# Kernel optimization log

Hardware: AMD Instinct MI355X
Metric: run time of the kernel (lower is better)

The kernel has to match this reference:

```python
import jax, jax.numpy as jnp
import numpy as np

DIM = 1024
HEADS = 16
HEAD_DIM = DIM // HEADS          # 64
ROT_DIM = max(16, HEAD_DIM // 2) # 32 (already even)
B, S = 1, 2048


def _linear_params(key, scale=0.02):
    w = jax.random.normal(key, (DIM, DIM), dtype=jnp.float32) * scale
    b = jnp.zeros((DIM,), dtype=jnp.float32)
    return w, b


def setup_inputs() -> dict:
    key = jax.random.key(0)
    ks = jax.random.split(key, 16)
    real = jax.random.normal(ks[0], (B, S, DIM), dtype=jnp.float32)
    imag = jax.random.normal(ks[1], (B, S, DIM), dtype=jnp.float32)
    Wq_r, bq_r = _linear_params(ks[2])
    Wk_r, bk_r = _linear_params(ks[3])
    Wv_r, bv_r = _linear_params(ks[4])
    Wq_i, bq_i = _linear_params(ks[5])
    Wk_i, bk_i = _linear_params(ks[6])
    Wv_i, bv_i = _linear_params(ks[7])
    Wo_r, bo_r = _linear_params(ks[8])
    Wo_i, bo_i = _linear_params(ks[9])
    phase_shifts = jax.random.normal(ks[10], (HEADS, HEAD_DIM), dtype=jnp.float32) * 0.02
    # entanglement init: 0.8*I + 0.1 on super/sub diagonal + 0.1 corners
    ent = np.eye(HEADS, dtype=np.float32) * 0.8
    ent += np.diag(np.ones(HEADS - 1, dtype=np.float32) * 0.1, k=1)
    ent += np.diag(np.ones(HEADS - 1, dtype=np.float32) * 0.1, k=-1)
    ent[0, -1] = 0.1
    ent[-1, 0] = 0.1
    entanglement_matrix = jnp.asarray(ent)
    exponent = np.arange(0, ROT_DIM, 2, dtype=np.float64) / ROT_DIM
    rotary_freqs = jnp.asarray((10000.0 ** (-exponent)).astype(np.float32))
    return {
        'real': real, 'imag': imag,
        'Wq_r': Wq_r, 'bq_r': bq_r, 'Wk_r': Wk_r, 'bk_r': bk_r,
        'Wv_r': Wv_r, 'bv_r': bv_r, 'Wq_i': Wq_i, 'bq_i': bq_i,
        'Wk_i': Wk_i, 'bk_i': bk_i, 'Wv_i': Wv_i, 'bv_i': bv_i,
        'Wo_r': Wo_r, 'bo_r': bo_r, 'Wo_i': Wo_i, 'bo_i': bo_i,
        'phase_shifts': phase_shifts,
        'entanglement_matrix': entanglement_matrix,
        'rotary_freqs': rotary_freqs,
        'interference_strength': jnp.float32(0.0),
        'attention_temperature': jnp.float32(0.0),
        'circle_epsilon': jnp.float32(-2.0),
    }


def _proj(x, W, b):
    # nn.Linear: x @ W^T + b, then split heads -> [B,H,S,Dh]
    y = x @ W.T + b
    return y.reshape(B, S, HEADS, HEAD_DIM).transpose(0, 2, 1, 3)


def _rope(x, cos, sin):
    # x: [B,H,S,Dh]; interleaved pairs rotated over first ROT_DIM dims
    xr, xp = x[..., :ROT_DIM], x[..., ROT_DIM:]
    x1, x2 = xr[..., 0::2], xr[..., 1::2]          # [B,H,S,ROT_DIM//2]
    o1 = x1 * cos - x2 * sin
    o2 = x1 * sin + x2 * cos
    out = jnp.stack([o1, o2], axis=-1).reshape(x.shape[:-1] + (ROT_DIM,))
    return jnp.concatenate([out, xp], axis=-1)


def reference(real, imag, Wq_r, bq_r, Wk_r, bk_r, Wv_r, bv_r,
              Wq_i, bq_i, Wk_i, bk_i, Wv_i, bv_i,
              Wo_r, bo_r, Wo_i, bo_i,
              phase_shifts, entanglement_matrix, rotary_freqs,
              interference_strength, attention_temperature, circle_epsilon):
    q_r = _proj(real, Wq_r, bq_r)
    k_r = _proj(real, Wk_r, bk_r)
    v_r = _proj(real, Wv_r, bv_r)
    q_i = _proj(imag, Wq_i, bq_i)
    k_i = _proj(imag, Wk_i, bk_i)
    v_i = _proj(imag, Wv_i, bv_i)

    # rotary embeddings
    pos = jnp.arange(S, dtype=jnp.float32)
    angles = jnp.outer(pos, rotary_freqs)              # [S, ROT_DIM//2]
    cos = jnp.cos(angles)[None, None]                  # [1,1,S,ROT_DIM//2]
    sin = jnp.sin(angles)[None, None]
    q_r = _rope(q_r, cos, sin); k_r = _rope(k_r, cos, sin)
    q_i = _rope(q_i, cos, sin); k_i = _rope(k_i, cos, sin)

    # entanglement mixing across heads
    q_r = jnp.einsum('bhsd,hx->bxsd', q_r, entanglement_matrix)
    q_i = jnp.einsum('bhsd,hx->bxsd', q_i, entanglement_matrix)
    k_r = jnp.einsum('bhsd,hx->bxsd', k_r, entanglement_matrix)
    k_i = jnp.einsum('bhsd,hx->bxsd', k_i, entanglement_matrix)

    # per-head learned phase shift
    pc = jnp.cos(phase_shifts)[None, :, None, :]       # [1,H,1,Dh]
    ps = jnp.sin(phase_shifts)[None, :, None, :]
    q_r, q_i = q_r * pc - q_i * ps, q_r * ps + q_i * pc
    k_r, k_i = k_r * pc - k_i * ps, k_r * ps + k_i * pc

    # complex attention scores (Karatsuba, as in HAKMEMComplexOperations)
    scale = 1.0 / np.sqrt(HEAD_DIM)
    k1 = jnp.einsum('bhsd,bhtd->bhst', q_r, k_r)
    k2 = jnp.einsum('bhsd,bhtd->bhst', q_i, k_i)
    k3 = jnp.einsum('bhsd,bhtd->bhst', q_r + q_i, k_r + k_i)
    attn_r = (k1 - k2) * scale
    attn_i = (k3 - k1 - k2) * scale

    eps = jax.nn.sigmoid(circle_epsilon) * 0.03
    ar = attn_r + eps * attn_i
    ai = attn_i - eps * attn_r
    attn_mag = jnp.sqrt(ar * ar + ai * ai + 1e-6)

    causal = jnp.triu(jnp.ones((S, S), dtype=bool), k=1)[None, None]
    attn_mag = jnp.where(causal, -jnp.inf, attn_mag)

    temp = jnp.clip(jnp.exp(attention_temperature), 0.1, None)
    strength = jax.nn.sigmoid(interference_strength)
    attn = jax.nn.softmax(attn_mag * strength / temp, axis=-1)
    attn = jnp.nan_to_num(attn)

    # complex_matmul(attn, 0, v_r, v_i) -> (attn@v_r, attn@v_i)
    out_r = jnp.einsum('bhst,bhtd->bhsd', attn, v_r)
    out_i = jnp.einsum('bhst,bhtd->bhsd', attn, v_i)
    out_r = out_r.transpose(0, 2, 1, 3).reshape(B, S, DIM)
    out_i = out_i.transpose(0, 2, 1, 3).reshape(B, S, DIM)
    out_r = out_r @ Wo_r.T + bo_r
    out_i = out_i @ Wo_i.T + bo_i
    return out_r, out_i
```

## Files before the change

kernel.cpp:

```cpp
#include <hip/hip_runtime.h>
#include <cstddef>
#include <cstdint>
#include <math.h>

#define S_LEN 2048
#define DIM 1024
#define NH 16
#define HD 64

typedef __attribute__((ext_vector_type(8))) short bf16x8;
typedef __attribute__((ext_vector_type(8))) unsigned short u16x8;
typedef __attribute__((ext_vector_type(4))) float f32x4;

__device__ inline unsigned short f2bf(float x) {
  union { float f; unsigned u; } v; v.f = x;
  unsigned r = v.u + 0x7FFFu + ((v.u >> 16) & 1u);
  return (unsigned short)(r >> 16);
}
__device__ inline float bf2f(unsigned short x) {
  union { unsigned u; float f; } v; v.u = ((unsigned)x) << 16; return v.f;
}

#define GLOAD_LDS16(g, l)                                              \
  __builtin_amdgcn_global_load_lds(                                    \
      (const __attribute__((address_space(1))) void*)(g),              \
      (__attribute__((address_space(3))) void*)(l), 16, 0, 0)

struct ConvBatch {
  const float* src[10];
  unsigned short* dst[10];
  int n[10];
};

__global__ __launch_bounds__(256) void conv_kernel(ConvBatch cb)
{
  const int y = blockIdx.y;
  const int i = (blockIdx.x * 256 + threadIdx.x) * 8;
  if (i >= cb.n[y]) return;
  const float* s = cb.src[y];
  float4 a = *(const float4*)(s + i);
  float4 b = *(const float4*)(s + i + 4);
  u16x8 o;
  o[0] = f2bf(a.x); o[1] = f2bf(a.y); o[2] = f2bf(a.z); o[3] = f2bf(a.w);
  o[4] = f2bf(b.x); o[5] = f2bf(b.y); o[6] = f2bf(b.z); o[7] = f2bf(b.w);
  *(u16x8*)(cb.dst[y] + i) = o;
}

struct BGemm {
  const unsigned short* A[6];
  const unsigned short* W[6];
  const float* bias[6];
  void* C[6];
  int mode[6];
};

__global__ __launch_bounds__(256) void gemm_mfma_kernel(BGemm gb)
{
  constexpr int K = DIM;
  const int z = blockIdx.z;
  const unsigned short* __restrict__ A = gb.A[z];
  const unsigned short* __restrict__ W = gb.W[z];
  const float* __restrict__ bias = gb.bias[z];
  const int mode = gb.mode[z];

  __shared__ __align__(16) unsigned short As[128 * 32];
  __shared__ __align__(16) unsigned short Ws[128 * 32];

  const int t    = threadIdx.x;
  const int lane = t & 63;
  const int w    = t >> 6;
  const int wm   = w >> 1, wn = w & 1;
  const int quad = lane >> 4, lcol = lane & 15;
  const int m0   = blockIdx.y * 128;
  const int n0   = blockIdx.x * 128;

  const int srow = t >> 2;
  const int sk8  = (t & 3) * 8;

  f32x4 acc[4][4];
#pragma unroll
  for (int i = 0; i < 4; i++)
#pragma unroll
    for (int j = 0; j < 4; j++)
#pragma unroll
      for (int r = 0; r < 4; r++) acc[i][j][r] = 0.f;

  for (int k0 = 0; k0 < K; k0 += 32) {
    __syncthreads();
#pragma unroll
    for (int p = 0; p < 2; p++) {
      const unsigned short* ga = A + (size_t)(m0 + p * 64 + srow) * K + k0 + sk8;
      GLOAD_LDS16(ga, As + (size_t)(p * 256 + w * 64) * 8);
      const unsigned short* gw = W + (size_t)(n0 + p * 64 + srow) * K + k0 + sk8;
      GLOAD_LDS16(gw, Ws + (size_t)(p * 256 + w * 64) * 8);
    }
    __syncthreads();

    bf16x8 af[4], bfr[4];
#pragma unroll
    for (int mi = 0; mi < 4; mi++)
      af[mi] = *(const bf16x8*)&As[(wm * 64 + mi * 16 + lcol) * 32 + quad * 8];
#pragma unroll
    for (int ni = 0; ni < 4; ni++)
      bfr[ni] = *(const bf16x8*)&Ws[(wn * 64 + ni * 16 + lcol) * 32 + quad * 8];
#pragma unroll
    for (int mi = 0; mi < 4; mi++)
#pragma unroll
      for (int ni = 0; ni < 4; ni++)
        acc[mi][ni] = __builtin_amdgcn_mfma_f32_16x16x32_bf16(af[mi], bfr[ni], acc[mi][ni], 0, 0, 0);
  }

#pragma unroll
  for (int mi = 0; mi < 4; mi++) {
#pragma unroll
    for (int ni = 0; ni < 4; ni++) {
#pragma unroll
      for (int r = 0; r < 4; r++) {
        const int grow = m0 + wm * 64 + mi * 16 + quad * 4 + r;
        const int gcol = n0 + wn * 64 + ni * 16 + lcol;
        const float v = acc[mi][ni][r] + bias[gcol];
        if (mode == 0) {
          ((float*)gb.C[z])[(size_t)grow * DIM + gcol] = v;
        } else if (mode == 1) {
          const int hh = gcol >> 6, d = gcol & 63;
          ((unsigned short*)gb.C[z])[((size_t)hh * S_LEN + grow) * HD + d] = f2bf(v);
        } else {
          const int hh = gcol >> 6, d = gcol & 63;
          ((unsigned short*)gb.C[z])[((size_t)hh * HD + d) * S_LEN + grow] = f2bf(v);
        }
      }
    }
  }
}

__global__ __launch_bounds__(256) void rope_kernel(
    unsigned short* q_r, unsigned short* k_r,
    unsigned short* q_i, unsigned short* k_i,
    const float* __restrict__ freqs)
{
  const int gid = blockIdx.x * 256 + threadIdx.x;
  const int j  = gid & 15;
  const int s  = (gid >> 4) & (S_LEN - 1);
  const int h  = (gid >> 15) & (NH - 1);
  const int tz = gid >> 19;
  unsigned short* buf = (tz == 0) ? q_r : (tz == 1) ? k_r : (tz == 2) ? q_i : k_i;

  const float ang = (float)s * freqs[j];
  float sn, cs;
  sincosf(ang, &sn, &cs);

  const size_t base = ((size_t)h * S_LEN + s) * HD + 2 * j;
  ushort2 xv = *(const ushort2*)(buf + base);
  const float x1 = bf2f(xv.x), x2 = bf2f(xv.y);
  ushort2 ov;
  ov.x = f2bf(x1 * cs - x2 * sn);
  ov.y = f2bf(x1 * sn + x2 * cs);
  *(ushort2*)(buf + base) = ov;
}

__global__ __launch_bounds__(256) void entangle_kernel(
    const unsigned short* __restrict__ qr_in, const unsigned short* __restrict__ qi_in,
    unsigned short* __restrict__ qr_out, unsigned short* __restrict__ qi_out,
    const unsigned short* __restrict__ kr_in, const unsigned short* __restrict__ ki_in,
    unsigned short* __restrict__ kr_out, unsigned short* __restrict__ ki_out,
    const float* __restrict__ E, const float* __restrict__ phase)
{
  const int z = blockIdx.z;
  const unsigned short* inR = z ? kr_in : qr_in;
  const unsigned short* inI = z ? ki_in : qi_in;
  unsigned short* outR = z ? kr_out : qr_out;
  unsigned short* outI = z ? ki_out : qi_out;

  __shared__ float Es[NH * NH];
  const int t = threadIdx.x;
  Es[t] = E[t];
  __syncthreads();

  const int idx = blockIdx.x * 256 + t;
  const int s = idx >> 6;
  const int d = idx & 63;

  float vr[NH], vi[NH];
#pragma unroll
  for (int h = 0; h < NH; h++) {
    const size_t off = ((size_t)h * S_LEN + s) * HD + d;
    vr[h] = bf2f(inR[off]);
    vi[h] = bf2f(inI[off]);
  }

#pragma unroll
  for (int x = 0; x < NH; x++) {
    float er = 0.f, ei = 0.f;
#pragma unroll
    for (int h = 0; h < NH; h++) {
      const float e = Es[h * NH + x];
      er += vr[h] * e;
      ei += vi[h] * e;
    }
    const float ph = phase[x * HD + d];
    float ps, pc;
    sincosf(ph, &ps, &pc);
    const size_t off = ((size_t)x * S_LEN + s) * HD + d;
    outR[off] = f2bf(er * pc - ei * ps);
    outI[off] = f2bf(er * ps + ei * pc);
  }
}

#define LDK 72

__global__ __launch_bounds__(256) void flash_mfma_kernel(
    const unsigned short* __restrict__ Qr, const unsigned short* __restrict__ Qi,
    const unsigned short* __restrict__ Kr, const unsigned short* __restrict__ Ki,
    const unsigned short* __restrict__ VtR, const unsigned short* __restrict__ VtI,
    unsigned short* __restrict__ Or, unsigned short* __restrict__ Oi,
    const float* __restrict__ p_is, const float* __restrict__ p_at,
    const float* __restrict__ p_ce)
{
  __shared__ __align__(16) unsigned short Krs[64 * LDK];
  __shared__ __align__(16) unsigned short Kis[64 * LDK];
  __shared__ __align__(16) unsigned short VTr[64 * LDK];
  __shared__ __align__(16) unsigned short VTi[64 * LDK];
  __shared__ __align__(16) unsigned short Ps [64 * LDK];

  const int t    = threadIdx.x;
  const int lane = t & 63;
  const int w    = t >> 6;
  const int quad = lane >> 4;
  const int lcol = lane & 15;
  const int h    = blockIdx.y;
  const int itile = 31 - blockIdx.x;
  const int i0   = itile * 64;
  const int ntiles = itile + 1;

  const float strength = 1.f / (1.f + expf(-p_is[0]));
  const float temp     = fmaxf(expf(p_at[0]), 0.1f);
  const float cfac     = strength / temp;
  const float eps      = 0.03f / (1.f + expf(-p_ce[0]));
  const float scale    = 0.125f;

  const int srow = t >> 3;
  const int sd0  = (t & 7) * 8;

  bf16x8 qrf[2], qif[2];
  {
    const int qrow = i0 + w * 16 + lcol;
    const size_t base = ((size_t)h * S_LEN + qrow) * HD;
#pragma unroll
    for (int ks = 0; ks < 2; ks++) {
      qrf[ks] = *(const bf16x8*)(Qr + base + ks * 32 + quad * 8);
      qif[ks] = *(const bf16x8*)(Qi + base + ks * 32 + quad * 8);
    }
  }

  float lsum[4] = {0.f, 0.f, 0.f, 0.f};
  f32x4 aOr[4], aOi[4];
#pragma unroll
  for (int c = 0; c < 4; c++)
#pragma unroll
    for (int r = 0; r < 4; r++) { aOr[c][r] = 0.f; aOi[c][r] = 0.f; }

  bf16x8 pk[2], pki[2], pv[2], pvi[2];

  {
    const size_t kb = ((size_t)h * S_LEN) * HD;
#pragma unroll
    for (int it = 0; it < 2; it++) {
      const int row = srow + it * 32;
      pk [it] = *(const bf16x8*)(Kr  + kb + (size_t)row * HD + sd0);
      pki[it] = *(const bf16x8*)(Ki  + kb + (size_t)row * HD + sd0);
      pv [it] = *(const bf16x8*)(VtR + ((size_t)h * HD + row) * S_LEN + sd0);
      pvi[it] = *(const bf16x8*)(VtI + ((size_t)h * HD + row) * S_LEN + sd0);
    }
  }

  for (int jt = 0; jt < ntiles; jt++) {
    __syncthreads();
#pragma unroll
    for (int it = 0; it < 2; it++) {
      const int row = srow + it * 32;
      *(bf16x8*)&Krs[row * LDK + sd0] = pk [it];
      *(bf16x8*)&Kis[row * LDK + sd0] = pki[it];
      *(bf16x8*)&VTr[row * LDK + sd0] = pv [it];
      *(bf16x8*)&VTi[row * LDK + sd0] = pvi[it];
    }
    __syncthreads();

    if (jt + 1 < ntiles) {
      const int j0n = (jt + 1) * 64;
      const size_t kb = ((size_t)h * S_LEN + j0n) * HD;
#pragma unroll
      for (int it = 0; it < 2; it++) {
        const int row = srow + it * 32;
        pk [it] = *(const bf16x8*)(Kr  + kb + (size_t)row * HD + sd0);
        pki[it] = *(const bf16x8*)(Ki  + kb + (size_t)row * HD + sd0);
        pv [it] = *(const bf16x8*)(VtR + ((size_t)h * HD + row) * S_LEN + j0n + sd0);
        pvi[it] = *(const bf16x8*)(VtI + ((size_t)h * HD + row) * S_LEN + j0n + sd0);
      }
    }

    f32x4 k1[4], k2[4], kx[4];
#pragma unroll
    for (int c = 0; c < 4; c++)
#pragma unroll
      for (int r = 0; r < 4; r++) { k1[c][r] = 0.f; k2[c][r] = 0.f; kx[c][r] = 0.f; }
#pragma unroll
    for (int ks = 0; ks < 2; ks++) {
#pragma unroll
      for (int c = 0; c < 4; c++) {
        const int off = (c * 16 + lcol) * LDK + ks * 32 + quad * 8;
        bf16x8 krf = *(const bf16x8*)&Krs[off];
        bf16x8 kif = *(const bf16x8*)&Kis[off];
        k1[c] = __builtin_amdgcn_mfma_f32_16x16x32_bf16(qrf[ks], krf, k1[c], 0, 0, 0);
        k2[c] = __builtin_amdgcn_mfma_f32_16x16x32_bf16(qif[ks], kif, k2[c], 0, 0, 0);
        kx[c] = __builtin_amdgcn_mfma_f32_16x16x32_bf16(qrf[ks], kif, kx[c], 0, 0, 0);
        kx[c] = __builtin_amdgcn_mfma_f32_16x16x32_bf16(qif[ks], krf, kx[c], 0, 0, 0);
      }
    }

    const bool diag = (jt == ntiles - 1);
    const int j0 = jt * 64;
#pragma unroll
    for (int r = 0; r < 4; r++) {
      const int prow = (w * 16 + quad * 4 + r) * LDK;
      float rs = 0.f;
#pragma unroll
      for (int c = 0; c < 4; c++) {
        const float ar_ = (k1[c][r] - k2[c][r]) * scale;
        const float ai_ = kx[c][r] * scale;
        const float arr = ar_ + eps * ai_;
        const float aii = ai_ - eps * ar_;
        const float mag = sqrtf(arr * arr + aii * aii + 1e-6f);
        float p = __expf(mag * cfac);
        if (diag) {
          const int gi = i0 + w * 16 + quad * 4 + r;
          const int gj = j0 + c * 16 + lcol;
          if (gj > gi) p = 0.f;
        }
        Ps[prow + c * 16 + lcol] = f2bf(p);
        rs += p;
      }
      lsum[r] += rs;
    }

#pragma unroll
    for (int ks = 0; ks < 2; ks++) {
      bf16x8 pf = *(const bf16x8*)&Ps[(w * 16 + lcol) * LDK + ks * 32 + quad * 8];
#pragma unroll
      for (int c = 0; c < 4; c++) {
        const int off = (c * 16 + lcol) * LDK + ks * 32 + quad * 8;
        bf16x8 vrf = *(const bf16x8*)&VTr[off];
        bf16x8 vif = *(const bf16x8*)&VTi[off];
        aOr[c] = __builtin_amdgcn_mfma_f32_16x16x32_bf16(pf, vrf, aOr[c], 0, 0, 0);
        aOi[c] = __builtin_amdgcn_mfma_f32_16x16x32_bf16(pf, vif, aOi[c], 0, 0, 0);
      }
    }
  }

  float inv[4];
#pragma unroll
  for (int r = 0; r < 4; r++) {
    float rs = lsum[r];
#pragma unroll
    for (int off = 1; off < 16; off <<= 1)
      rs += __shfl_xor(rs, off, 16);
    inv[r] = 1.f / rs;
  }

#pragma unroll
  for (int c = 0; c < 4; c++) {
#pragma unroll
    for (int r = 0; r < 4; r++) {
      const int row = i0 + w * 16 + quad * 4 + r;
      const int col = h * HD + c * 16 + lcol;
      Or[(size_t)row * DIM + col] = f2bf(aOr[c][r] * inv[r]);
      Oi[(size_t)row * DIM + col] = f2bf(aOi[c][r] * inv[r]);
    }
  }
}

extern "C" void kernel_launch(void* const* d_in, const int* in_sizes, int n_in,
                              void* d_out, int out_size, void* d_ws, size_t ws_size,
                              hipStream_t stream)
{
  const float* real = (const float*)d_in[0];
  const float* imag = (const float*)d_in[1];
  const float* Wq_r = (const float*)d_in[2];
  const float* bq_r = (const float*)d_in[3];
  const float* Wk_r = (const float*)d_in[4];
  const float* bk_r = (const float*)d_in[5];
  const float* Wv_r = (const float*)d_in[6];
  const float* bv_r = (const float*)d_in[7];
  const float* Wq_i = (const float*)d_in[8];
  const float* bq_i = (const float*)d_in[9];
  const float* Wk_i = (const float*)d_in[10];
  const float* bk_i = (const float*)d_in[11];
  const float* Wv_i = (const float*)d_in[12];
  const float* bv_i = (const float*)d_in[13];
  const float* Wo_r = (const float*)d_in[14];
  const float* bo_r = (const float*)d_in[15];
  const float* Wo_i = (const float*)d_in[16];
  const float* bo_i = (const float*)d_in[17];
  const float* phase = (const float*)d_in[18];
  const float* ent   = (const float*)d_in[19];
  const float* freqs = (const float*)d_in[20];
  const float* p_is  = (const float*)d_in[21];
  const float* p_at  = (const float*)d_in[22];
  const float* p_ce  = (const float*)d_in[23];

  unsigned short* ws = (unsigned short*)d_ws;
  const size_t SL = (size_t)S_LEN * DIM;
  const size_t WL = (size_t)DIM * DIM;

  unsigned short* realb = ws;
  unsigned short* imagb = realb + SL;
  unsigned short* Wb    = imagb + SL;
  unsigned short* q_r   = Wb + 8 * WL;
  unsigned short* k_r   = q_r + SL;
  unsigned short* v_r   = k_r + SL;
  unsigned short* q_i   = v_r + SL;
  unsigned short* k_i   = q_i + SL;
  unsigned short* v_i   = k_i + SL;
  unsigned short* Qr    = v_i + SL;
  unsigned short* Qi    = Qr + SL;
  unsigned short* Kr    = Qi + SL;
  unsigned short* Ki    = Kr + SL;
  unsigned short* O_r   = q_r;
  unsigned short* O_i   = q_i;

  float* out_r = (float*)d_out;
  float* out_i = out_r + SL;

  ConvBatch cb;
  cb.src[0] = real; cb.dst[0] = realb; cb.n[0] = (int)SL;
  cb.src[1] = imag; cb.dst[1] = imagb; cb.n[1] = (int)SL;
  const float* wsrc[8] = {Wq_r, Wk_r, Wv_r, Wq_i, Wk_i, Wv_i, Wo_r, Wo_i};
  for (int i = 0; i < 8; i++) {
    cb.src[2 + i] = wsrc[i];
    cb.dst[2 + i] = Wb + (size_t)i * WL;
    cb.n[2 + i] = (int)WL;
  }
  conv_kernel<<<dim3(1024, 10), dim3(256), 0, stream>>>(cb);

  BGemm g1;
  g1.A[0] = realb; g1.A[1] = realb; g1.A[2] = realb;
  g1.A[3] = imagb; g1.A[4] = imagb; g1.A[5] = imagb;
  for (int i = 0; i < 6; i++) g1.W[i] = Wb + (size_t)i * WL;
  g1.bias[0] = bq_r; g1.bias[1] = bk_r; g1.bias[2] = bv_r;
  g1.bias[3] = bq_i; g1.bias[4] = bk_i; g1.bias[5] = bv_i;
  g1.C[0] = q_r; g1.C[1] = k_r; g1.C[2] = v_r;
  g1.C[3] = q_i; g1.C[4] = k_i; g1.C[5] = v_i;
  g1.mode[0] = 1; g1.mode[1] = 1; g1.mode[2] = 2;
  g1.mode[3] = 1; g1.mode[4] = 1; g1.mode[5] = 2;
  gemm_mfma_kernel<<<dim3(8, 16, 6), dim3(256), 0, stream>>>(g1);

  rope_kernel<<<dim3(8192), dim3(256), 0, stream>>>(q_r, k_r, q_i, k_i, freqs);

  entangle_kernel<<<dim3(512, 1, 2), dim3(256), 0, stream>>>(
      q_r, q_i, Qr, Qi, k_r, k_i, Kr, Ki, ent, phase);

  flash_mfma_kernel<<<dim3(32, NH), dim3(256), 0, stream>>>(
      Qr, Qi, Kr, Ki, v_r, v_i, O_r, O_i, p_is, p_at, p_ce);

  BGemm g2 = {};
  g2.A[0] = O_r; g2.A[1] = O_i;
  g2.W[0] = Wb + 6 * WL; g2.W[1] = Wb + 7 * WL;
  g2.bias[0] = bo_r; g2.bias[1] = bo_i;
  g2.C[0] = out_r; g2.C[1] = out_i;
  g2.mode[0] = 0; g2.mode[1] = 0;
  gemm_mfma_kernel<<<dim3(8, 16, 2), dim3(256), 0, stream>>>(g2);
}
```

Baseline: 338.2 us.

## Pair short and long causal tiles in flash grid and simplify magnitude math

The flash attention launch becomes a 1D grid of 512 blocks. The first 256 blocks take query tiles 0..15 across all heads, and the second 256 take the mirrored tiles 31..16, so a CU that holds one block from each half gets a balanced total of causal work. The epsilon rotation of the score is also folded algebraically: the magnitude is computed as sqrt((a²+b²)·scale²·(1+eps²)+1e-6), which drops several multiplies per score element. The balancing depends on how the hardware assigns blocks to CUs. The fold changes floating-point rounding slightly.

After: 304.3 us. 1.11x faster.

```diff
diff --git a/kernel.cpp b/kernel.cpp
--- a/kernel.cpp
+++ b/kernel.cpp
@@ -227,8 +227,12 @@
   const int w    = t >> 6;
   const int quad = lane >> 4;
   const int lcol = lane & 15;
-  const int h    = blockIdx.y;
-  const int itile = 31 - blockIdx.x;
+
+  const int L    = blockIdx.x;
+  const int c    = L & 255;
+  const int h    = c & 15;
+  const int base = c >> 4;
+  const int itile = (L >> 8) ? (31 - base) : base;
   const int i0   = itile * 64;
   const int ntiles = itile + 1;
 
@@ -236,7 +240,7 @@
   const float temp     = fmaxf(expf(p_at[0]), 0.1f);
   const float cfac     = strength / temp;
   const float eps      = 0.03f / (1.f + expf(-p_ce[0]));
-  const float scale    = 0.125f;
+  const float c2       = 0.015625f * (1.f + eps * eps);
 
   const int srow = t >> 3;
   const int sd0  = (t & 7) * 8;
@@ -244,20 +248,20 @@
   bf16x8 qrf[2], qif[2];
   {
     const int qrow = i0 + w * 16 + lcol;
-    const size_t base = ((size_t)h * S_LEN + qrow) * HD;
+    const size_t base_q = ((size_t)h * S_LEN + qrow) * HD;
 #pragma unroll
     for (int ks = 0; ks < 2; ks++) {
-      qrf[ks] = *(const bf16x8*)(Qr + base + ks * 32 + quad * 8);
-      qif[ks] = *(const bf16x8*)(Qi + base + ks * 32 + quad * 8);
+      qrf[ks] = *(const bf16x8*)(Qr + base_q + ks * 32 + quad * 8);
+      qif[ks] = *(const bf16x8*)(Qi + base_q + ks * 32 + quad * 8);
     }
   }
 
   float lsum[4] = {0.f, 0.f, 0.f, 0.f};
   f32x4 aOr[4], aOi[4];
 #pragma unroll
-  for (int c = 0; c < 4; c++)
-#pragma unroll
-    for (int r = 0; r < 4; r++) { aOr[c][r] = 0.f; aOi[c][r] = 0.f; }
+  for (int cc = 0; cc < 4; cc++)
+#pragma unroll
+    for (int r = 0; r < 4; r++) { aOr[cc][r] = 0.f; aOi[cc][r] = 0.f; }
 
   bf16x8 pk[2], pki[2], pv[2], pvi[2];
 
@@ -300,20 +304,20 @@
 
     f32x4 k1[4], k2[4], kx[4];
 #pragma unroll
-    for (int c = 0; c < 4; c++)
-#pragma unroll
-      for (int r = 0; r < 4; r++) { k1[c][r] = 0.f; k2[c][r] = 0.f; kx[c][r] = 0.f; }
+    for (int cc = 0; cc < 4; cc++)
+#pragma unroll
+      for (int r = 0; r < 4; r++) { k1[cc][r] = 0.f; k2[cc][r] = 0.f; kx[cc][r] = 0.f; }
 #pragma unroll
     for (int ks = 0; ks < 2; ks++) {
 #pragma unroll
-      for (int c = 0; c < 4; c++) {
-        const int off = (c * 16 + lcol) * LDK + ks * 32 + quad * 8;
+      for (int cc = 0; cc < 4; cc++) {
+        const int off = (cc * 16 + lcol) * LDK + ks * 32 + quad * 8;
         bf16x8 krf = *(const bf16x8*)&Krs[off];
         bf16x8 kif = *(const bf16x8*)&Kis[off];
-        k1[c] = __builtin_amdgcn_mfma_f32_16x16x32_bf16(qrf[ks], krf, k1[c], 0, 0, 0);
-        k2[c] = __builtin_amdgcn_mfma_f32_16x16x32_bf16(qif[ks], kif, k2[c], 0, 0, 0);
-        kx[c] = __builtin_amdgcn_mfma_f32_16x16x32_bf16(qrf[ks], kif, kx[c], 0, 0, 0);
-        kx[c] = __builtin_amdgcn_mfma_f32_16x16x32_bf16(qif[ks], krf, kx[c], 0, 0, 0);
+        k1[cc] = __builtin_amdgcn_mfma_f32_16x16x32_bf16(qrf[ks], krf, k1[cc], 0, 0, 0);
+        k2[cc] = __builtin_amdgcn_mfma_f32_16x16x32_bf16(qif[ks], kif, k2[cc], 0, 0, 0);
+        kx[cc] = __builtin_amdgcn_mfma_f32_16x16x32_bf16(qrf[ks], kif, kx[cc], 0, 0, 0);
+        kx[cc] = __builtin_amdgcn_mfma_f32_16x16x32_bf16(qif[ks], krf, kx[cc], 0, 0, 0);
       }
     }
 
@@ -324,19 +328,18 @@
       const int prow = (w * 16 + quad * 4 + r) * LDK;
       float rs = 0.f;
 #pragma unroll
-      for (int c = 0; c < 4; c++) {
-        const float ar_ = (k1[c][r] - k2[c][r]) * scale;
-        const float ai_ = kx[c][r] * scale;
-        const float arr = ar_ + eps * ai_;
-        const float aii = ai_ - eps * ar_;
-        const float mag = sqrtf(arr * arr + aii * aii + 1e-6f);
+      for (int cc = 0; cc < 4; cc++) {
+        const float a = k1[cc][r] - k2[cc][r];
+        const float b = kx[cc][r];
+        const float u = fmaf(b, b, a * a);
+        const float mag = sqrtf(fmaf(u, c2, 1e-6f));
         float p = __expf(mag * cfac);
         if (diag) {
           const int gi = i0 + w * 16 + quad * 4 + r;
-          const int gj = j0 + c * 16 + lcol;
+          const int gj = j0 + cc * 16 + lcol;
           if (gj > gi) p = 0.f;
         }
-        Ps[prow + c * 16 + lcol] = f2bf(p);
+        Ps[prow + cc * 16 + lcol] = f2bf(p);
         rs += p;
       }
       lsum[r] += rs;
@@ -346,12 +349,12 @@
     for (int ks = 0; ks < 2; ks++) {
       bf16x8 pf = *(const bf16x8*)&Ps[(w * 16 + lcol) * LDK + ks * 32 + quad * 8];
 #pragma unroll
-      for (int c = 0; c < 4; c++) {
-        const int off = (c * 16 + lcol) * LDK + ks * 32 + quad * 8;
+      for (int cc = 0; cc < 4; cc++) {
+        const int off = (cc * 16 + lcol) * LDK + ks * 32 + quad * 8;
         bf16x8 vrf = *(const bf16x8*)&VTr[off];
         bf16x8 vif = *(const bf16x8*)&VTi[off];
-        aOr[c] = __builtin_amdgcn_mfma_f32_16x16x32_bf16(pf, vrf, aOr[c], 0, 0, 0);
-        aOi[c] = __builtin_amdgcn_mfma_f32_16x16x32_bf16(pf, vif, aOi[c], 0, 0, 0);
+        aOr[cc] = __builtin_amdgcn_mfma_f32_16x16x32_bf16(pf, vrf, aOr[cc], 0, 0, 0);
+        aOi[cc] = __builtin_amdgcn_mfma_f32_16x16x32_bf16(pf, vif, aOi[cc], 0, 0, 0);
       }
     }
   }
@@ -367,13 +370,13 @@
   }
 
 #pragma unroll
-  for (int c = 0; c < 4; c++) {
+  for (int cc = 0; cc < 4; cc++) {
 #pragma unroll
     for (int r = 0; r < 4; r++) {
       const int row = i0 + w * 16 + quad * 4 + r;
-      const int col = h * HD + c * 16 + lcol;
-      Or[(size_t)row * DIM + col] = f2bf(aOr[c][r] * inv[r]);
-      Oi[(size_t)row * DIM + col] = f2bf(aOi[c][r] * inv[r]);
+      const int col = h * HD + cc * 16 + lcol;
+      Or[(size_t)row * DIM + col] = f2bf(aOr[cc][r] * inv[r]);
+      Oi[(size_t)row * DIM + col] = f2bf(aOi[cc][r] * inv[r]);
     }
   }
 }
@@ -458,7 +461,7 @@
   entangle_kernel<<<dim3(512, 1, 2), dim3(256), 0, stream>>>(
       q_r, q_i, Qr, Qi, k_r, k_i, Kr, Ki, ent, phase);
 
-  flash_mfma_kernel<<<dim3(32, NH), dim3(256), 0, stream>>>(
+  flash_mfma_kernel<<<dim3(512), dim3(256), 0, stream>>>(
       Qr, Qi, Kr, Ki, v_r, v_i, O_r, O_i, p_is, p_at, p_ce);
 
   BGemm g2 = {};
```
